# Optimization experiments

Measured on AMD Instinct MI355X. Metric: run time of the kernel, lower is better.

## Reference

```python
import jax, jax.numpy as jnp
import numpy as np

BS, CH, T = 128, 16, 12288
RED = 6          # mini_window_temporal_reduction_factor
N = CH * RED     # 96 mini-windows
K = 5            # top-k selected mini-windows
NCLS = 5
LATENT = (T // 16) * 8  # hypernet flatten dim = 6144


def _conv1d(x, w, b=None):
    # x: [B,C,L], w: [O,I,ks] -> [B,O,L-ks+1]
    out = jax.lax.conv_general_dilated(x, w, (1,), 'VALID', dimension_numbers=('NCH', 'OIH', 'NCH'))
    return out if b is None else out + b[None, :, None]


def _same_reflect(x, w, b):
    p = (w.shape[-1] - 1) // 2
    return _conv1d(jnp.pad(x, ((0, 0), (0, 0), (p, p)), mode='reflect'), w, b)


def _leaky(z):
    return jnp.where(z >= 0, z, 0.01 * z)


def _pool(x, f, op):
    L = x.shape[-1] // f  # floor, drop remainder (matches torch pooling)
    xr = x[..., :L * f].reshape(x.shape[:-1] + (L, f))
    return op(xr, -1)


def setup_inputs() -> dict:
    key = jax.random.key(0)
    ks = jax.random.split(key, 18)
    s = 0.05
    return {
        'x': jax.random.normal(ks[0], (BS, CH, T), jnp.float32),
        'epoch': 0,
        # hypernet conv blocks (padding='same', reflect)
        'hw1': jax.random.normal(ks[1], (32, CH, 7), jnp.float32) * s,
        'hb1': jnp.zeros((32,), jnp.float32),
        'hw2': jax.random.normal(ks[2], (64, 32, 7), jnp.float32) * s,
        'hb2': jnp.zeros((64,), jnp.float32),
        'hw3': jax.random.normal(ks[3], (8, 64, 7), jnp.float32) * s,
        'hb3': jnp.zeros((8,), jnp.float32),
        'hl1': jax.random.normal(ks[4], (N, LATENT), jnp.float32) * s,  # Linear(latent->N), no bias
        'hl2': jax.random.normal(ks[5], (N, N), jnp.float32) * s,       # Linear(N->N), no bias
        # GroupedIdxConv1D: per-group Conv1d(1, 64, ks=15); bias only for group 0
        'gw': jax.random.normal(ks[6], (CH, 64, 15), jnp.float32) * s,
        'gb0': jax.random.normal(ks[7], (64,), jnp.float32) * s,
        # encoder convs 1,2
        'ew2': jax.random.normal(ks[8], (128, 64, 7), jnp.float32) * s,
        'eb2': jnp.zeros((128,), jnp.float32),
        'ew3': jax.random.normal(ks[9], (128, 128, 7), jnp.float32) * s,
        'eb3': jnp.zeros((128,), jnp.float32),
        # classifier
        'cw': jax.random.normal(ks[10], (NCLS, 128), jnp.float32) * s,
        'cb': jnp.zeros((NCLS,), jnp.float32),
    }


def reference(x, epoch, hw1, hb1, hw2, hb2, hw3, hb3, hl1, hl2, gw, gb0, ew2, eb2, ew3, eb3, cw, cb):
    # Eval-mode forward (active sampling, no Gumbel noise, hard top-k one-hot, dropout off)
    bs = x.shape[0]
    # ---- hypernet ----
    h = _pool(_leaky(_same_reflect(x, hw1, hb1)), 4, jnp.mean)
    h = _pool(_leaky(_same_reflect(h, hw2, hb2)), 4, jnp.mean)
    h = jnp.tanh(_same_reflect(h, hw3, hb3)).reshape(bs, -1)
    logits = _leaky(h @ hl1.T) @ hl2.T  # [bs, N]
    # ---- hard top-k sampling (bmm with one-hot == gather rows) ----
    _, idx = jax.lax.top_k(logits, K)                      # [bs, K]
    x_r = x.reshape(bs, N, -1)                             # [bs, N, T']
    sel = jnp.take_along_axis(x_r, idx[:, :, None], axis=1)  # [bs, K, T']
    gidx = idx // RED                                      # ExG channel group per mini-window
    # ---- GroupedIdxConv1D: per-element kernel gather + conv + sum over K ----
    ksz = gw.shape[-1]
    Lout = sel.shape[-1] - ksz + 1
    windows = jnp.stack([sel[..., i:i + Lout] for i in range(ksz)], axis=-1)  # [bs,K,Lout,ksz]
    kernels = gw[gidx]                                     # [bs,K,64,ksz]
    z = jnp.einsum('bkls,bkos->bol', windows, kernels)     # conv + sum over channel axis K
    n0 = (gidx == 0).sum(1).astype(z.dtype)                # bias only for group 0 elements
    z = z + n0[:, None, None] * gb0[None, :, None]
    # ---- encoder tail ----
    z = _pool(_leaky(z), 4, jnp.max)
    z = _pool(_leaky(_conv1d(z, ew2, eb2)), 4, jnp.max)
    z = _conv1d(z, ew3, eb3).mean(-1)                      # AdaptiveAvgPool1d(1) -> [bs,128]
    # ---- classifier ----
    return jax.nn.log_softmax(z @ cw.T + cb, -1)           # [bs, NCLS]
```

## Files before the change

### kernel.cpp

```cpp
#include <hip/hip_runtime.h>
#include <hip/hip_bf16.h>
#include <math.h>

typedef unsigned short u16;
typedef __attribute__((ext_vector_type(8))) short short8;
typedef __attribute__((ext_vector_type(4))) float floatx4;

__device__ __forceinline__ float lk(float v){ return v >= 0.f ? v : 0.01f*v; }
__device__ __forceinline__ u16 f2b(float f){
    __hip_bfloat16 h = __float2bfloat16(f);
    return *reinterpret_cast<u16*>(&h);
}
__device__ __forceinline__ int refl(int t, int L){
    return t < 0 ? -t : (t >= L ? 2*L-2-t : t);
}

__global__ __launch_bounds__(256) void k_prep(const float* __restrict__ hw1,
        const float* __restrict__ hw2, const float* __restrict__ ew2,
        const float* __restrict__ gw, u16* __restrict__ wb)
{
    int idx = blockIdx.x*256 + threadIdx.x;
    if (idx < 4096){
        int u = idx; int j=u&7; int o=(u>>3)&31; int kq=(u>>8)&3; int s=u>>10;
        int tap = 2*s + (kq>>1); int ic = (kq&1)*8 + j;
        wb[idx] = (tap<7) ? f2b(hw1[(o*16+ic)*7+tap]) : (u16)0;
    } else if (idx < 18432){
        int u = idx - 4096; int j=u&7; int o=(u>>3)&63; int kq=(u>>9)&3; int s=u>>11;
        wb[idx] = f2b(hw2[(o*32 + kq*8 + j)*7 + s]);
    } else if (idx < 75776){
        int u = idx - 18432; int j=u&7; int o=(u>>3)&127; int kq=(u>>10)&3; int s=u>>12;
        int ih = s/7, tap = s-ih*7;
        wb[idx] = f2b(ew2[(o*64 + ih*32 + kq*8 + j)*7 + tap]);
    } else if (idx < 92160){
        int u = idx - 75776; int j=u&7; int o=(u>>3)&63; int tb=(u>>9)&1; int gi=u>>10;
        int tap = tb*8 + j;
        wb[idx] = (tap<15) ? f2b(gw[gi*960 + o*15 + tap]) : (u16)0;
    }
}

__global__ __launch_bounds__(256,4) void k_hconv1(const float* __restrict__ x,
        const u16* __restrict__ wb1, const float* __restrict__ bias,
        u16* __restrict__ h1)
{
    __shared__ __align__(16) u16 xs[2][264*24];
    __shared__ __align__(16) u16 ob[2][64*32];
    int b = blockIdx.x / 24, pb = blockIdx.x % 24;
    int tid = threadIdx.x;
    const float* xb = x + (size_t)b*16*12288;
    int wv = tid >> 6, lane = tid & 63;
    int m = lane & 15, kq = lane >> 4;
    int ohalf = wv & 1, thalf = wv >> 1;
    int o = ohalf*16 + m;

    short8 wfr[4];
    #pragma unroll
    for (int s=0;s<4;s++)
        wfr[s] = *reinterpret_cast<const short8*>(&wb1[(((s*4+kq)*32)+o)*8]);
    float bv = bias[o];

    float rg0[16]; float rgx;
    int exrow = 256 + (tid>>4), exch = tid & 15;

#define LOADTILE(G0) { \
        int t0 = refl((G0) - 3 + tid, 12288); \
        _Pragma("unroll") \
        for (int ic=0;ic<16;ic++) rg0[ic] = xb[(size_t)ic*12288 + t0]; \
        if (tid < 128){ \
            int t1 = refl((G0) - 3 + exrow, 12288); \
            rgx = xb[(size_t)exch*12288 + t1]; \
        } \
        __builtin_amdgcn_sched_barrier(0); }

#define WRITETILE(BUF) { \
        short8 p0, p1; \
        _Pragma("unroll") \
        for (int j=0;j<8;j++){ p0[j] = (short)f2b(rg0[j]); p1[j] = (short)f2b(rg0[8+j]); } \
        *reinterpret_cast<short8*>(&xs[BUF][tid*24])     = p0; \
        *reinterpret_cast<short8*>(&xs[BUF][tid*24 + 8]) = p1; \
        if (tid < 128) xs[BUF][exrow*24 + exch] = f2b(rgx); }

#define COMPUTETILE(BUF) { \
        floatx4 acc[8]; \
        _Pragma("unroll") \
        for (int i=0;i<8;i++) acc[i] = (floatx4){0.f,0.f,0.f,0.f}; \
        int tb0 = thalf*128; \
        _Pragma("unroll") \
        for (int sub=0; sub<8; sub++){ \
            int tb = tb0 + sub*16; \
            _Pragma("unroll") \
            for (int s=0;s<4;s++){ \
                int tap = 2*s + (kq>>1); \
                short8 xfr = *reinterpret_cast<const short8*>( \
                                &xs[BUF][(tb + m + tap)*24 + (kq&1)*8]); \
                acc[sub] = __builtin_amdgcn_mfma_f32_16x16x32_bf16(xfr, wfr[s], acc[sub], 0,0,0); \
            } \
        } \
        _Pragma("unroll") \
        for (int sub=0; sub<8; sub++){ \
            float sum = lk(acc[sub][0]+bv) + lk(acc[sub][1]+bv) \
                      + lk(acc[sub][2]+bv) + lk(acc[sub][3]+bv); \
            ob[BUF][(thalf*32 + sub*4 + kq)*32 + o] = f2b(sum*0.25f); \
        } }

#define STORETILE(BUF, TILE) { \
        short8 v = *reinterpret_cast<const short8*>(&ob[BUF][tid*8]); \
        *reinterpret_cast<short8*>(&h1[((size_t)b*3072 + (TILE)*64)*32 + tid*8]) = v; }

    int g0 = pb*512;
    LOADTILE(g0);
    WRITETILE(0);
    __syncthreads();
    LOADTILE(g0 + 256);
    COMPUTETILE(0);
    WRITETILE(1);
    __syncthreads();
    STORETILE(0, pb*2);
    COMPUTETILE(1);
    __syncthreads();
    STORETILE(1, pb*2 + 1);

#undef LOADTILE
#undef WRITETILE
#undef COMPUTETILE
#undef STORETILE
}

__global__ __launch_bounds__(256,4) void k_hconv2(const u16* __restrict__ h1,
        const u16* __restrict__ wb2, const float* __restrict__ bias,
        float* __restrict__ h2)
{
    __shared__ __align__(16) u16 xs[2][198*40];
    int b = blockIdx.x >> 3, tile = blockIdx.x & 7;
    int tid = threadIdx.x;
    int wv = tid >> 6, lane = tid & 63;
    int m = lane & 15, kq = lane >> 4;
    int o = wv*16 + m;

    short8 wfr[7];
    #pragma unroll
    for (int s=0;s<7;s++)
        wfr[s] = *reinterpret_cast<const short8*>(&wb2[(((s*4+kq)*64)+o)*8]);
    float bv = bias[o];

    short8 rgA[3], rgX;

#define LOADH(HALF) { \
        int gh = tile*384 + (HALF)*192 - 3; \
        _Pragma("unroll") \
        for (int cc=0;cc<3;cc++){ \
            int c = tid + cc*256; \
            int row = c >> 2, q = c & 3; \
            int t = refl(gh + row, 3072); \
            rgA[cc] = *reinterpret_cast<const short8*>(&h1[((size_t)b*3072 + t)*32 + q*8]); \
        } \
        if (tid < 24){ \
            int c = 768 + tid; \
            int row = c >> 2, q = c & 3; \
            int t = refl(gh + row, 3072); \
            rgX = *reinterpret_cast<const short8*>(&h1[((size_t)b*3072 + t)*32 + q*8]); \
        } \
        __builtin_amdgcn_sched_barrier(0); }

#define WRITEH(BUF) { \
        _Pragma("unroll") \
        for (int cc=0;cc<3;cc++){ \
            int c = tid + cc*256; \
            *reinterpret_cast<short8*>(&xs[BUF][(c>>2)*40 + (c&3)*8]) = rgA[cc]; \
        } \
        if (tid < 24){ \
            int c = 768 + tid; \
            *reinterpret_cast<short8*>(&xs[BUF][(c>>2)*40 + (c&3)*8]) = rgX; \
        } }

#define COMPUTEH(BUF, HALF) { \
        floatx4 acc[12]; \
        _Pragma("unroll") \
        for (int i=0;i<12;i++) acc[i] = (floatx4){0.f,0.f,0.f,0.f}; \
        for (int sub=0; sub<12; sub++){ \
            int tb = sub*16; \
            _Pragma("unroll") \
            for (int s=0;s<7;s++){ \
                short8 xfr = *reinterpret_cast<const short8*>( \
                                &xs[BUF][(tb + m + s)*40 + kq*8]); \
                acc[sub] = __builtin_amdgcn_mfma_f32_16x16x32_bf16(xfr, wfr[s], acc[sub], 0,0,0); \
            } \
        } \
        _Pragma("unroll") \
        for (int sub=0; sub<12; sub++){ \
            float sum = lk(acc[sub][0]+bv) + lk(acc[sub][1]+bv) \
                      + lk(acc[sub][2]+bv) + lk(acc[sub][3]+bv); \
            h2[((size_t)b*768 + tile*96 + (HALF)*48 + sub*4 + kq)*64 + o] = sum*0.25f; \
        } }

    LOADH(0);
    WRITEH(0);
    __syncthreads();
    LOADH(1);
    COMPUTEH(0, 0);
    WRITEH(1);
    __syncthreads();
    COMPUTEH(1, 1);

#undef LOADH
#undef WRITEH
#undef COMPUTEH
}

__global__ __launch_bounds__(256) void k_hconv3(const float* __restrict__ h2,
        const float* __restrict__ w, const float* __restrict__ bias,
        float* __restrict__ latent)
{
    __shared__ float xs[64*201];
    int b = blockIdx.x >> 2, tile = blockIdx.x & 3;
    int g0 = tile*192;
    int tid = threadIdx.x;
    for (int idx = tid; idx < 198*64; idx += 256){
        int jj = idx >> 6, ic = idx & 63;
        int t = refl(g0 + jj - 3, 768);
        xs[ic*201 + jj] = h2[((size_t)b*768 + t)*64 + ic];
    }
    __syncthreads();
    int c = tid >> 5, run = tid & 31;
    int p0 = run*6;
    float acc[6];
    #pragma unroll
    for (int l=0;l<6;l++) acc[l] = 0.f;
    for (int ic=0; ic<64; ic++){
        const float* wp = w + (c*64+ic)*7;
        float wr[7];
        #pragma unroll
        for (int s=0;s<7;s++) wr[s] = wp[s];
        const float* xr = xs + ic*201 + p0;
        float xw[12];
        #pragma unroll
        for (int j=0;j<12;j++) xw[j] = xr[j];
        #pragma unroll
        for (int s=0;s<7;s++)
            #pragma unroll
            for (int l=0;l<6;l++) acc[l] += wr[s]*xw[l+s];
    }
    float bv = bias[c];
    float* op = latent + (size_t)b*6144 + c*768 + g0 + p0;
    #pragma unroll
    for (int l=0;l<6;l++) op[l] = tanhf(acc[l] + bv);
}

__global__ __launch_bounds__(256) void k_lin1(const float* __restrict__ latent,
        const float* __restrict__ hl1, float* __restrict__ t1)
{
    __shared__ float ls[6144];
    int b = blockIdx.x / 6, ntile = blockIdx.x % 6;
    int tid = threadIdx.x;
    const float4* lp = reinterpret_cast<const float4*>(latent + (size_t)b*6144);
    float4* lsv = reinterpret_cast<float4*>(ls);
    for (int i = tid; i < 1536; i += 256) lsv[i] = lp[i];
    __syncthreads();
    int wv = tid >> 6, lane = tid & 63;
    #pragma unroll
    for (int nn=0; nn<4; nn++){
        int n = ntile*16 + wv*4 + nn;
        const float4* wp = reinterpret_cast<const float4*>(hl1 + (size_t)n*6144);
        float s = 0.f;
        #pragma unroll
        for (int j=0;j<24;j++){
            float4 q = wp[lane + 64*j];
            float4 l4 = lsv[lane + 64*j];
            s += l4.x*q.x + l4.y*q.y + l4.z*q.z + l4.w*q.w;
        }
        #pragma unroll
        for (int off=32; off; off>>=1) s += __shfl_down(s, off);
        if (lane==0) t1[b*96+n] = lk(s);
    }
}

__global__ __launch_bounds__(128) void k_topk(const float* __restrict__ t1,
        const float* __restrict__ hl2, int* __restrict__ idxb, float* __restrict__ n0f)
{
    __shared__ float lg[96];
    int b = blockIdx.x, n = threadIdx.x;
    if (n < 96){
        float s = 0.f;
        const float* tp = t1 + b*96;
        const float* wp = hl2 + n*96;
        for (int m=0;m<96;m++) s += tp[m]*wp[m];
        lg[n] = s;
    }
    __syncthreads();
    if (threadIdx.x == 0){
        unsigned long long u0=0ull, u1=0ull;
        float n0 = 0.f;
        for (int k=0;k<5;k++){
            float best = -3.4e38f; int bi = 0;
            for (int m=0;m<96;m++){
                bool used = m<64 ? ((u0>>m)&1ull) : ((u1>>(m-64))&1ull);
                if (!used && lg[m] > best){ best = lg[m]; bi = m; }
            }
            if (bi<64) u0 |= 1ull<<bi; else u1 |= 1ull<<(bi-64);
            idxb[b*5+k] = bi;
            if (bi < 6) n0 += 1.f;
        }
        n0f[b] = n0;
    }
}

__global__ __launch_bounds__(256,3) void k_gconv(const float* __restrict__ x,
        const int* __restrict__ idxb, const float* __restrict__ n0f,
        const u16* __restrict__ gwb, const float* __restrict__ gb0,
        u16* __restrict__ zp)
{
    __shared__ __align__(16) u16 xs[5][8][536];
    __shared__ int nidx[5];
    __shared__ float n0s;
    int b = blockIdx.x >> 2, qc = blockIdx.x & 3;
    int tid = threadIdx.x;
    int p0g = qc*512;

    if (tid < 5) nidx[tid] = idxb[b*5 + tid];
    if (tid == 5) n0s = n0f[b];
    __syncthreads();

    for (int cch = tid; cch < 5*134; cch += 256){
        int k = cch / 134, q = cch - k*134;
        const float* xrow = x + (size_t)b*196608 + (size_t)nidx[k]*2048;
        int base = p0g + q*4;
        u16 vb[4];
        if (base + 3 <= 2047){
            float4 a = *reinterpret_cast<const float4*>(xrow + base);
            vb[0]=f2b(a.x); vb[1]=f2b(a.y); vb[2]=f2b(a.z); vb[3]=f2b(a.w);
        } else {
            #pragma unroll
            for (int jj=0;jj<4;jj++){
                int ii = base+jj; if (ii > 2047) ii = 2047;
                vb[jj] = f2b(xrow[ii]);
            }
        }
        #pragma unroll
        for (int jj=0;jj<4;jj++){
            int gof = q*4 + jj;
            #pragma unroll
            for (int r=0;r<8;r++){
                int i = gof - r;
                if (i >= 0 && i < 528) xs[k][r][i] = vb[jj];
            }
        }
    }

    int wv = tid >> 6, lane = tid & 63;
    int m = lane & 15, kq = lane >> 4;
    int o = wv*16 + m;

    short8 wfr[3];
    #pragma unroll
    for (int c=0;c<3;c++){
        int kk = 2*c + (kq>>1);
        int kkc = kk < 5 ? kk : 4;
        int gi = nidx[kkc] / 6;
        short8 f = *reinterpret_cast<const short8*>(
                        &gwb[(((gi*2 + (kq&1))*64)+o)*8]);
        if (kk >= 5) f = (short8)(short)0;
        wfr[c] = f;
    }
    float bv = n0s * gb0[o];
    __syncthreads();

    int rr = m & 7, ibase = (m & 8) + (kq & 1)*8;
    for (int g8 = 0; g8 < 4; ++g8){
        floatx4 acc[8];
        #pragma unroll
        for (int i=0;i<8;i++) acc[i] = (floatx4){0.f,0.f,0.f,0.f};
        #pragma unroll
        for (int s8=0; s8<8; ++s8){
            int P = (g8*8 + s8)*16;
            #pragma unroll
            for (int c=0;c<3;c++){
                int kk = 2*c + (kq>>1);
                int kkc = kk < 5 ? kk : 4;
                short8 af = *reinterpret_cast<const short8*>(&xs[kkc][rr][P + ibase]);
                acc[s8] = __builtin_amdgcn_mfma_f32_16x16x32_bf16(af, wfr[c], acc[s8], 0,0,0);
            }
        }
        #pragma unroll
        for (int s8=0; s8<8; ++s8){
            int sub = g8*8 + s8;
            int Q = qc*128 + sub*4 + kq;
            if (Q < 508){
                float mx = fmaxf(fmaxf(lk(acc[s8][0]+bv), lk(acc[s8][1]+bv)),
                                 fmaxf(lk(acc[s8][2]+bv), lk(acc[s8][3]+bv)));
                zp[((size_t)b*508 + Q)*64 + o] = f2b(mx);
            }
        }
    }
}

__global__ __launch_bounds__(256,1) void k_econv2(const u16* __restrict__ zp,
        const u16* __restrict__ wbe, const float* __restrict__ bias,
        float* __restrict__ p2)
{
    __shared__ __align__(16) u16 xs[118*72];
    int b = blockIdx.x / 5, tile = blockIdx.x % 5;
    int tid = threadIdx.x;
    for (int c = tid; c < 118*8; c += 256){
        int row = c >> 3, q = c & 7;
        int t = tile*100 + row; if (t > 507) t = 507;
        *reinterpret_cast<short8*>(&xs[row*72 + q*8]) =
            *reinterpret_cast<const short8*>(&zp[((size_t)b*508 + t)*64 + q*8]);
    }
    __syncthreads();
    int wv = tid >> 6, lane = tid & 63;
    int m = lane & 15, kq = lane >> 4;
    for (int half=0; half<2; half++){
        int ot = wv + 4*half;
        int o = ot*16 + m;
        short8 wfr[14];
        #pragma unroll
        for (int s=0;s<14;s++)
            wfr[s] = *reinterpret_cast<const short8*>(&wbe[(((s*4+kq)*128)+o)*8]);
        floatx4 acc[7];
        #pragma unroll
        for (int i=0;i<7;i++) acc[i] = (floatx4){0.f,0.f,0.f,0.f};
        #pragma unroll
        for (int sub=0; sub<7; sub++){
            #pragma unroll
            for (int s=0;s<14;s++){
                int tap = s%7, ih = s/7;
                short8 xfr = *reinterpret_cast<const short8*>(
                                &xs[(sub*16 + m + tap)*72 + ih*32 + kq*8]);
                acc[sub] = __builtin_amdgcn_mfma_f32_16x16x32_bf16(xfr, wfr[s], acc[sub], 0,0,0);
            }
        }
        float bv = bias[o];
        #pragma unroll
        for (int sub=0; sub<7; sub++){
            int pidx = sub*4 + kq;
            if (pidx < 25){
                float mx = fmaxf(fmaxf(lk(acc[sub][0]+bv), lk(acc[sub][1]+bv)),
                                 fmaxf(lk(acc[sub][2]+bv), lk(acc[sub][3]+bv)));
                p2[((size_t)b*125 + tile*25 + pidx)*128 + o] = mx;
            }
        }
    }
}

__global__ __launch_bounds__(128) void k_tail(const float* __restrict__ p2,
        const float* __restrict__ w, const float* __restrict__ bias,
        const float* __restrict__ cw, const float* __restrict__ cb,
        float* __restrict__ out)
{
    __shared__ float ss[7][128];
    __shared__ float ft[128];
    __shared__ float lgs[5];
    int b = blockIdx.x, tid = threadIdx.x;

    {
        const float* pb = p2 + (size_t)b*125*128 + tid;
        float first6[6], last6[6];
        float c = 0.f;
        #pragma unroll
        for (int t=0;t<6;t++){ float v = pb[(size_t)t*128]; first6[t]=v; c+=v; }
        for (int t=6;t<119;t++) c += pb[(size_t)t*128];
        #pragma unroll
        for (int t=0;t<6;t++) last6[t] = pb[(size_t)(119+t)*128];
        ss[0][tid] = c;
        #pragma unroll
        for (int s=0;s<6;s++){ c = c - first6[s] + last6[s]; ss[s+1][tid] = c; }
    }
    __syncthreads();

    {
        const float* wp = w + (size_t)tid*896;
        float s = 0.f;
        for (int ic=0; ic<128; ic++){
            #pragma unroll
            for (int tp=0; tp<7; tp++)
                s += wp[ic*7+tp]*ss[tp][ic];
        }
        ft[tid] = s*(1.f/119.f) + bias[tid];
    }
    __syncthreads();

    if (tid < 5){
        float lg = cb[tid];
        const float* wp = cw + tid*128;
        for (int o=0;o<128;o++) lg += ft[o]*wp[o];
        lgs[tid] = lg;
    }
    __syncthreads();
    if (tid == 0){
        float mx = -3.4e38f;
        for (int c=0;c<5;c++) mx = fmaxf(mx, lgs[c]);
        float se = 0.f;
        for (int c=0;c<5;c++) se += expf(lgs[c]-mx);
        float lse = mx + logf(se);
        for (int c=0;c<5;c++) out[b*5+c] = lgs[c]-lse;
    }
}

extern "C" void kernel_launch(void* const* d_in, const int* in_sizes, int n_in,
                              void* d_out, int out_size, void* d_ws, size_t ws_size,
                              hipStream_t stream)
{
    const float* x   = (const float*)d_in[0];
    const float* hw1 = (const float*)d_in[2];
    const float* hb1 = (const float*)d_in[3];
    const float* hw2 = (const float*)d_in[4];
    const float* hb2 = (const float*)d_in[5];
    const float* hw3 = (const float*)d_in[6];
    const float* hb3 = (const float*)d_in[7];
    const float* hl1 = (const float*)d_in[8];
    const float* hl2 = (const float*)d_in[9];
    const float* gw  = (const float*)d_in[10];
    const float* gb0 = (const float*)d_in[11];
    const float* ew2 = (const float*)d_in[12];
    const float* eb2 = (const float*)d_in[13];
    const float* ew3 = (const float*)d_in[14];
    const float* eb3 = (const float*)d_in[15];
    const float* cw  = (const float*)d_in[16];
    const float* cb  = (const float*)d_in[17];
    float* out = (float*)d_out;

    float* f       = (float*)d_ws;
    float* latent  = f;
    float* t1      = f + 786432;
    int*   idxb    = (int*)(f + 806432);
    float* n0f     = f + 808432;
    u16*   zpb     = (u16*)(f + 810000);
    u16*   wb      = (u16*)(f + 2900000);
    float* h2      = f + 3932160;
    float* p2      = f + 5000000;
    u16*   h1b     = (u16*)(f + 10223616);

    k_prep<<<360, 256, 0, stream>>>(hw1, hw2, ew2, gw, wb);
    k_hconv1<<<3072, 256, 0, stream>>>(x, wb, hb1, h1b);
    k_hconv2<<<1024, 256, 0, stream>>>(h1b, wb + 4096, hb2, h2);
    k_hconv3<<<512, 256, 0, stream>>>(h2, hw3, hb3, latent);
    k_lin1<<<768, 256, 0, stream>>>(latent, hl1, t1);
    k_topk<<<128, 128, 0, stream>>>(t1, hl2, idxb, n0f);
    k_gconv<<<512, 256, 0, stream>>>(x, idxb, n0f, wb + 75776, gb0, zpb);
    k_econv2<<<640, 256, 0, stream>>>(zpb, wb + 18432, eb2, p2);
    k_tail<<<128, 128, 0, stream>>>(p2, ew3, eb3, cw, cb, out);
}
```

Baseline: 358.9 us.

## Make hconv1 persistent over six tiles and reuse A-fragments across output tiles

k_hconv1 now runs 1024 blocks, and each block loops over six 256-step time tiles with a double-buffered load/compute/store pipeline. Each wave covers all 32 output channels over a quarter of the tile, so one x fragment feeds two MFMAs. k_hconv2 likewise has each wave compute all 64 output channels for three sub-tiles, loading weights in two halves, so LDS input fragments are reused across four N-tiles. Launch bounds change to 3 for hconv2 and 2 for econv2. This cuts LDS reads per MFMA and block launch overhead, at the cost of more registers and lower occupancy.

```diff
diff --git a/kernel.cpp b/kernel.cpp
--- a/kernel.cpp
+++ b/kernel.cpp
@@ -44,19 +44,21 @@
 {
     __shared__ __align__(16) u16 xs[2][264*24];
     __shared__ __align__(16) u16 ob[2][64*32];
-    int b = blockIdx.x / 24, pb = blockIdx.x % 24;
+    int b = blockIdx.x >> 3, chunk = blockIdx.x & 7;
     int tid = threadIdx.x;
     const float* xb = x + (size_t)b*16*12288;
     int wv = tid >> 6, lane = tid & 63;
     int m = lane & 15, kq = lane >> 4;
-    int ohalf = wv & 1, thalf = wv >> 1;
-    int o = ohalf*16 + m;
-
-    short8 wfr[4];
+    int tq = wv;
+
+    short8 wfr[4][2];
     #pragma unroll
     for (int s=0;s<4;s++)
-        wfr[s] = *reinterpret_cast<const short8*>(&wb1[(((s*4+kq)*32)+o)*8]);
-    float bv = bias[o];
+        #pragma unroll
+        for (int oh=0;oh<2;oh++)
+            wfr[s][oh] = *reinterpret_cast<const short8*>(
+                            &wb1[(((s*4+kq)*32) + oh*16 + m)*8]);
+    float bv[2] = { bias[m], bias[16+m] };
 
     float rg0[16]; float rgx;
     int exrow = 256 + (tid>>4), exch = tid & 15;
@@ -80,44 +82,51 @@
         if (tid < 128) xs[BUF][exrow*24 + exch] = f2b(rgx); }
 
 #define COMPUTETILE(BUF) { \
-        floatx4 acc[8]; \
-        _Pragma("unroll") \
-        for (int i=0;i<8;i++) acc[i] = (floatx4){0.f,0.f,0.f,0.f}; \
-        int tb0 = thalf*128; \
-        _Pragma("unroll") \
-        for (int sub=0; sub<8; sub++){ \
-            int tb = tb0 + sub*16; \
+        floatx4 acc[4][2]; \
+        _Pragma("unroll") \
+        for (int i=0;i<4;i++){ acc[i][0] = (floatx4){0.f,0.f,0.f,0.f}; \
+                               acc[i][1] = (floatx4){0.f,0.f,0.f,0.f}; } \
+        _Pragma("unroll") \
+        for (int sub=0; sub<4; sub++){ \
+            int tb = tq*64 + sub*16; \
             _Pragma("unroll") \
             for (int s=0;s<4;s++){ \
                 int tap = 2*s + (kq>>1); \
                 short8 xfr = *reinterpret_cast<const short8*>( \
                                 &xs[BUF][(tb + m + tap)*24 + (kq&1)*8]); \
-                acc[sub] = __builtin_amdgcn_mfma_f32_16x16x32_bf16(xfr, wfr[s], acc[sub], 0,0,0); \
+                acc[sub][0] = __builtin_amdgcn_mfma_f32_16x16x32_bf16(xfr, wfr[s][0], acc[sub][0], 0,0,0); \
+                acc[sub][1] = __builtin_amdgcn_mfma_f32_16x16x32_bf16(xfr, wfr[s][1], acc[sub][1], 0,0,0); \
             } \
         } \
         _Pragma("unroll") \
-        for (int sub=0; sub<8; sub++){ \
-            float sum = lk(acc[sub][0]+bv) + lk(acc[sub][1]+bv) \
-                      + lk(acc[sub][2]+bv) + lk(acc[sub][3]+bv); \
-            ob[BUF][(thalf*32 + sub*4 + kq)*32 + o] = f2b(sum*0.25f); \
+        for (int sub=0; sub<4; sub++){ \
+            int p = tq*16 + sub*4 + kq; \
+            _Pragma("unroll") \
+            for (int oh=0; oh<2; oh++){ \
+                float sum = lk(acc[sub][oh][0]+bv[oh]) + lk(acc[sub][oh][1]+bv[oh]) \
+                          + lk(acc[sub][oh][2]+bv[oh]) + lk(acc[sub][oh][3]+bv[oh]); \
+                ob[BUF][p*32 + oh*16 + m] = f2b(sum*0.25f); \
+            } \
         } }
 
-#define STORETILE(BUF, TILE) { \
+#define STORETILE(BUF, TAU) { \
         short8 v = *reinterpret_cast<const short8*>(&ob[BUF][tid*8]); \
-        *reinterpret_cast<short8*>(&h1[((size_t)b*3072 + (TILE)*64)*32 + tid*8]) = v; }
-
-    int g0 = pb*512;
-    LOADTILE(g0);
+        *reinterpret_cast<short8*>(&h1[((size_t)b*3072 + (TAU)*64)*32 + tid*8]) = v; }
+
+    int tau0 = chunk*6;
+    LOADTILE(tau0*256);
     WRITETILE(0);
     __syncthreads();
-    LOADTILE(g0 + 256);
-    COMPUTETILE(0);
-    WRITETILE(1);
-    __syncthreads();
-    STORETILE(0, pb*2);
-    COMPUTETILE(1);
-    __syncthreads();
-    STORETILE(1, pb*2 + 1);
+    LOADTILE((tau0+1)*256);
+    #pragma unroll 1
+    for (int t=0; t<6; ++t){
+        int cur = t & 1;
+        COMPUTETILE(cur);
+        if (t < 5) WRITETILE(cur^1);
+        __syncthreads();
+        STORETILE(cur, tau0 + t);
+        if (t < 4) LOADTILE((tau0 + t + 2)*256);
+    }
 
 #undef LOADTILE
 #undef WRITETILE
@@ -125,7 +134,7 @@
 #undef STORETILE
 }
 
-__global__ __launch_bounds__(256,4) void k_hconv2(const u16* __restrict__ h1,
+__global__ __launch_bounds__(256,3) void k_hconv2(const u16* __restrict__ h1,
         const u16* __restrict__ wb2, const float* __restrict__ bias,
         float* __restrict__ h2)
 {
@@ -134,13 +143,10 @@
     int tid = threadIdx.x;
     int wv = tid >> 6, lane = tid & 63;
     int m = lane & 15, kq = lane >> 4;
-    int o = wv*16 + m;
-
-    short8 wfr[7];
+
+    float bv[4];
     #pragma unroll
-    for (int s=0;s<7;s++)
-        wfr[s] = *reinterpret_cast<const short8*>(&wb2[(((s*4+kq)*64)+o)*8]);
-    float bv = bias[o];
+    for (int nt=0;nt<4;nt++) bv[nt] = bias[nt*16 + m];
 
     short8 rgA[3], rgX;
 
@@ -173,23 +179,41 @@
         } }
 
 #define COMPUTEH(BUF, HALF) { \
-        floatx4 acc[12]; \
-        _Pragma("unroll") \
-        for (int i=0;i<12;i++) acc[i] = (floatx4){0.f,0.f,0.f,0.f}; \
-        for (int sub=0; sub<12; sub++){ \
-            int tb = sub*16; \
+        floatx4 acc[3][4]; \
+        _Pragma("unroll") \
+        for (int i=0;i<3;i++) \
             _Pragma("unroll") \
-            for (int s=0;s<7;s++){ \
-                short8 xfr = *reinterpret_cast<const short8*>( \
-                                &xs[BUF][(tb + m + s)*40 + kq*8]); \
-                acc[sub] = __builtin_amdgcn_mfma_f32_16x16x32_bf16(xfr, wfr[s], acc[sub], 0,0,0); \
+            for (int nt=0;nt<4;nt++) acc[i][nt] = (floatx4){0.f,0.f,0.f,0.f}; \
+        _Pragma("unroll") \
+        for (int nt2=0; nt2<2; ++nt2){ \
+            short8 wfr[7][2]; \
+            _Pragma("unroll") \
+            for (int s=0;s<7;s++) \
+                _Pragma("unroll") \
+                for (int c=0;c<2;c++) \
+                    wfr[s][c] = *reinterpret_cast<const short8*>( \
+                        &wb2[(((s*4+kq)*64) + (nt2*2+c)*16 + m)*8]); \
+            _Pragma("unroll") \
+            for (int i=0;i<3;i++){ \
+                int tb = (wv*3+i)*16; \
+                _Pragma("unroll") \
+                for (int s=0;s<7;s++){ \
+                    short8 xfr = *reinterpret_cast<const short8*>( \
+                                    &xs[BUF][(tb + m + s)*40 + kq*8]); \
+                    acc[i][nt2*2]   = __builtin_amdgcn_mfma_f32_16x16x32_bf16(xfr, wfr[s][0], acc[i][nt2*2],   0,0,0); \
+                    acc[i][nt2*2+1] = __builtin_amdgcn_mfma_f32_16x16x32_bf16(xfr, wfr[s][1], acc[i][nt2*2+1], 0,0,0); \
+                } \
             } \
         } \
         _Pragma("unroll") \
-        for (int sub=0; sub<12; sub++){ \
-            float sum = lk(acc[sub][0]+bv) + lk(acc[sub][1]+bv) \
-                      + lk(acc[sub][2]+bv) + lk(acc[sub][3]+bv); \
-            h2[((size_t)b*768 + tile*96 + (HALF)*48 + sub*4 + kq)*64 + o] = sum*0.25f; \
+        for (int i=0;i<3;i++){ \
+            int pooled = (wv*3+i)*4 + kq; \
+            _Pragma("unroll") \
+            for (int nt=0;nt<4;nt++){ \
+                float sum = lk(acc[i][nt][0]+bv[nt]) + lk(acc[i][nt][1]+bv[nt]) \
+                          + lk(acc[i][nt][2]+bv[nt]) + lk(acc[i][nt][3]+bv[nt]); \
+                h2[((size_t)b*768 + tile*96 + (HALF)*48 + pooled)*64 + nt*16 + m] = sum*0.25f; \
+            } \
         } }
 
     LOADH(0);
@@ -392,7 +416,7 @@
     }
 }
 
-__global__ __launch_bounds__(256,1) void k_econv2(const u16* __restrict__ zp,
+__global__ __launch_bounds__(256,2) void k_econv2(const u16* __restrict__ zp,
         const u16* __restrict__ wbe, const float* __restrict__ bias,
         float* __restrict__ p2)
 {
@@ -530,7 +554,7 @@
     u16*   h1b     = (u16*)(f + 10223616);
 
     k_prep<<<360, 256, 0, stream>>>(hw1, hw2, ew2, gw, wb);
-    k_hconv1<<<3072, 256, 0, stream>>>(x, wb, hb1, h1b);
+    k_hconv1<<<1024, 256, 0, stream>>>(x, wb, hb1, h1b);
     k_hconv2<<<1024, 256, 0, stream>>>(h1b, wb + 4096, hb2, h2);
     k_hconv3<<<512, 256, 0, stream>>>(h2, hw3, hb3, latent);
     k_lin1<<<768, 256, 0, stream>>>(latent, hl1, t1);
```

Measured after the change: 421.7 us. 17.5% more time.
